# Kernel tuning notes

Hardware: AMD Instinct MI355X
Metric: run time of the kernel (lower is better)

Reference implementation:

```python
import jax, jax.numpy as jnp
import numpy as np

B, S, H, DK, DM = 8, 2048, 8, 64, 512  # batch, seq, heads, head dim, model dim
NEG = jnp.float32(-2**31)  # fill value for float32 per source


def setup_inputs() -> dict:
    key = jax.random.key(0)
    ks = jax.random.split(key, 8)
    q = jax.random.normal(ks[0], (B, S, DK), dtype=jnp.float32)
    k = jax.random.normal(ks[1], (B, S, DK), dtype=jnp.float32)
    v = jax.random.normal(ks[2], (B, S, DK), dtype=jnp.float32)
    mask = jax.random.randint(ks[3], (B, S, S), 0, 2).astype(jnp.float32)
    # torch Linear params stored as [in, out] for x @ W + b
    Wq = jax.random.normal(ks[4], (DK, H * DK), dtype=jnp.float32) / np.sqrt(DK).astype(np.float32)
    bq = jax.random.normal(ks[5], (H * DK,), dtype=jnp.float32) * 0.02
    Wo = jax.random.normal(ks[6], (H * DK, DM), dtype=jnp.float32) / np.sqrt(H * DK).astype(np.float32)
    bo = jax.random.normal(ks[7], (DM,), dtype=jnp.float32) * 0.02
    return {"q": q, "k": k, "v": v, "mask": mask, "Wq": Wq, "bq": bq, "Wo": Wo, "bo": bo}


def reference(q, k, v, mask, Wq, bq, Wo, bo):
    # Faithful to the source BUG: linear_q projects q, k AND v.
    def proj(x):
        b, s, _ = x.shape
        return (x @ Wq + bq).reshape(b, s, H, DK).transpose(2, 0, 1, 3)  # [H,B,S,DK]

    qh, kh, vh = proj(q), proj(k), proj(v)
    e = jnp.einsum('hbqd,hbkd->hbqk', qh, kh) / np.float32(np.sqrt(DK))  # [H,B,Sq,Sk]
    # source fills where ((mask-1).bool()==False), i.e. where mask == 1.0
    e = jnp.where(mask[None] == 1.0, NEG, e)
    a = jax.nn.softmax(e, axis=-1)
    y = jnp.einsum('hbqk,hbkd->hbqd', a, vh)          # [H,B,Sq,DK]
    y = y.transpose(1, 2, 0, 3).reshape(B, S, H * DK)  # [B,Sq,H*DK]
    return y @ Wo + bo
```

## Files before the change

### kernel.cpp

```cpp
#include <hip/hip_runtime.h>
#include <hip/hip_bf16.h>

#define BB 8
#define SS 2048
#define HD 512
#define DM 512

typedef __attribute__((ext_vector_type(8))) short short8;
typedef __attribute__((ext_vector_type(4))) short short4v;
typedef __attribute__((ext_vector_type(4))) float floatx4;

__device__ __forceinline__ unsigned cvt_pk_bf16(float a, float b) {
    unsigned r;
    asm("v_cvt_pk_bf16_f32 %0, %1, %2" : "=v"(r) : "v"(a), "v"(b));
    return r;
}

__device__ __forceinline__ short f2bf(float f) {
    return (short)(cvt_pk_bf16(f, f) & 0xFFFFu);
}

__device__ __forceinline__ uint2 pack4bf(float a, float b, float cc, float d) {
    return uint2{cvt_pk_bf16(a, b), cvt_pk_bf16(cc, d)};
}

__device__ __forceinline__ short4v pack4bf_s4(float a, float b, float cc, float d) {
    uint2 u = pack4bf(a, b, cc, d);
    short4v s;
    __builtin_memcpy(&s, &u, 8);
    return s;
}

__device__ __forceinline__ void async_copy16(const short* g, short* l) {
    __builtin_amdgcn_global_load_lds(
        (const __attribute__((address_space(1))) void*)g,
        (__attribute__((address_space(3))) void*)l, 16, 0, 0);
}

__global__ void maskbits_prep_kernel(const float* __restrict__ mask,
                                     unsigned long long* __restrict__ bits,
                                     const float* __restrict__ Wq,
                                     const float* __restrict__ Wo,
                                     short* __restrict__ WqT,
                                     short* __restrict__ WoT) {
    int bid = blockIdx.x;
    if (bid >= 32768) {
        int idx = (bid - 32768) * 256 + threadIdx.x;
        if (idx < HD * 64) {
            int o = idx >> 6, i = idx & 63;
            WqT[idx] = f2bf(Wq[i * HD + o]);
        }
        int o = idx >> 9, i = idx & 511;
        WoT[idx] = f2bf(Wo[i * DM + o]);
        return;
    }
    int gw = bid * 4 + (threadIdx.x >> 6);
    int lane = threadIdx.x & 63;
    size_t base = (size_t)gw * 256;
    float4 v = *(const float4*)(mask + base + (size_t)lane * 4);
    unsigned long long nib =
        (v.x == 1.0f ? 1ull : 0ull) | (v.y == 1.0f ? 2ull : 0ull) |
        (v.z == 1.0f ? 4ull : 0ull) | (v.w == 1.0f ? 8ull : 0ull);
    unsigned long long word = nib << (4 * (lane & 15));
    word |= __shfl_xor(word, 1);
    word |= __shfl_xor(word, 2);
    word |= __shfl_xor(word, 4);
    word |= __shfl_xor(word, 8);
    if ((lane & 15) == 0) bits[gw * 4 + (lane >> 4)] = word;
}

__global__ __launch_bounds__(256, 2) void proj_kernel(
    const float* __restrict__ qA, const float* __restrict__ kA,
    const float* __restrict__ vA, const short* __restrict__ WqT,
    const float* __restrict__ bq, short* __restrict__ qh,
    short* __restrict__ khS, short* __restrict__ vI) {
    const int bid = blockIdx.x;
    const int part = bid >> 9, sub = bid & 511;

    __shared__ __align__(16) short LDSbuf[2 * 128 * 80];
    short* As = LDSbuf;
    short* Bs = LDSbuf + 128 * 80;
    short* Cs = LDSbuf;

    const int tid = threadIdx.x, lane = tid & 63, w = tid >> 6;
    const int c = lane & 15, Q = lane >> 4;
    const int wm = w >> 1, wn = w & 1;

    int n0, m0, bz = 0;
    const float* Af32 = nullptr;
    if (part < 2) {
        n0 = (sub & 3) * 128;
        m0 = (sub >> 2) * 128;
        Af32 = part ? kA : qA;
    } else {
        n0 = (sub & 15) * 128;
        int rest = sub >> 4;
        m0 = (rest & 3) * 128;
        bz = rest >> 2;
    }

#pragma unroll
    for (int it = 0; it < 4; ++it) {
        int chunk = it * 256 + tid;
        int row = chunk >> 3, c8 = chunk & 7;
        if (part < 2) {
            const float* Af = Af32 + (size_t)(m0 + row) * 64 + c8 * 8;
            float4 lo = *(const float4*)Af;
            float4 hi = *(const float4*)(Af + 4);
            uint2 p0 = pack4bf(lo.x, lo.y, lo.z, lo.w);
            uint2 p1 = pack4bf(hi.x, hi.y, hi.z, hi.w);
            *(uint4*)&As[row * 80 + c8 * 8] = uint4{p0.x, p0.y, p1.x, p1.y};
            *(uint4*)&Bs[row * 80 + c8 * 8] =
                *(const uint4*)(WqT + (size_t)(n0 + row) * 64 + c8 * 8);
        } else {
            *(uint4*)&As[row * 80 + c8 * 8] =
                *(const uint4*)(WqT + (size_t)(m0 + row) * 64 + c8 * 8);
            const float* Bf = vA + (size_t)bz * 131072 +
                              (size_t)(n0 + row) * 64 + c8 * 8;
            float4 lo = *(const float4*)Bf;
            float4 hi = *(const float4*)(Bf + 4);
            uint2 p0 = pack4bf(lo.x, lo.y, lo.z, lo.w);
            uint2 p1 = pack4bf(hi.x, hi.y, hi.z, hi.w);
            *(uint4*)&Bs[row * 80 + c8 * 8] = uint4{p0.x, p0.y, p1.x, p1.y};
        }
    }
    __syncthreads();

    floatx4 acc[4][4] = {};
#pragma unroll
    for (int ks = 0; ks < 2; ++ks) {
        short8 af[4], bf[4];
#pragma unroll
        for (int mt = 0; mt < 4; ++mt)
            af[mt] = *(const short8*)&As[(wm * 64 + mt * 16 + c) * 80 + ks * 32 + 8 * Q];
#pragma unroll
        for (int nt = 0; nt < 4; ++nt)
            bf[nt] = *(const short8*)&Bs[(wn * 64 + nt * 16 + c) * 80 + ks * 32 + 8 * Q];
#pragma unroll
        for (int mt = 0; mt < 4; ++mt)
#pragma unroll
            for (int nt = 0; nt < 4; ++nt)
                acc[mt][nt] = __builtin_amdgcn_mfma_f32_16x16x32_bf16(
                    af[mt], bf[nt], acc[mt][nt], 0, 0, 0);
    }
    __syncthreads();

#pragma unroll
    for (int mt = 0; mt < 4; ++mt)
#pragma unroll
        for (int nt = 0; nt < 4; ++nt) {
            int cl = wn * 64 + nt * 16 + c;
#pragma unroll
            for (int r = 0; r < 4; ++r) {
                int rl = wm * 64 + mt * 16 + 4 * Q + r;
                if (part == 0) {
                    float val = (acc[mt][nt][r] + bq[n0 + cl]) * 0.18033688011f;
                    Cs[rl * 128 + cl] = f2bf(val);
                } else if (part == 1) {
                    float val = acc[mt][nt][r] + bq[n0 + cl];
                    int d = cl & 63, hh = cl >> 6;
                    Cs[rl * 128 + hh * 64 + (((d >> 3) ^ (rl & 7)) * 8) + (d & 7)] =
                        f2bf(val);
                } else {
                    float val = acc[mt][nt][r] + bq[m0 + rl];
                    int d = rl & 63, hl = rl >> 6;
                    int Jl = cl >> 5, kp = cl & 31;
                    int j = 4 * ((kp >> 4) & 1) + (kp & 3);
                    int Qm = (kp >> 2) & 3;
                    int slotm = Qm ^ ((d >> 1) & 3);
                    Cs[(hl * 4 + Jl) * 2048 + d * 32 + slotm * 8 + j] = f2bf(val);
                }
            }
        }
    __syncthreads();

#pragma unroll
    for (int p = 0; p < 8; ++p) {
        int c2 = p * 256 + tid;
        uint4 vchunk;
        size_t gaddr;
        if (part == 0) {
            int row = c2 >> 4, off16 = c2 & 15;
            vchunk = *(const uint4*)&Cs[row * 128 + off16 * 8];
            gaddr = (size_t)(m0 + row) * HD + n0 + off16 * 8;
            *(uint4*)(qh + gaddr) = vchunk;
        } else if (part == 1) {
            int sp = c2 >> 3, off = c2 & 7;
            int s = sp >> 1, hh = sp & 1;
            vchunk = *(const uint4*)&Cs[s * 128 + hh * 64 + off * 8];
            int grow = m0 + s;
            int b = grow >> 11, sg = grow & 2047;
            int hg = (n0 >> 6) + hh;
            gaddr = ((size_t)(b * 8 + hg)) * 131072 + (size_t)sg * 64 + off * 8;
            *(uint4*)(khS + gaddr) = vchunk;
        } else {
            int region = c2 >> 8, off = c2 & 255;
            int hl = region >> 2, Jl = region & 3;
            vchunk = *(const uint4*)&Cs[region * 2048 + off * 8];
            int hg = (m0 >> 6) + hl;
            int Jg = (n0 >> 5) + Jl;
            gaddr = ((size_t)(bz * 8 + hg)) * 131072 + (size_t)Jg * 2048 + off * 8;
            *(uint4*)(vI + gaddr) = vchunk;
        }
    }
}

template <int SMODE, bool BIAS_ROW, bool A_F32, bool B_F32>
__global__ __launch_bounds__(256, 2) void gemm_bt(
    const void* __restrict__ A_, int lda, long sA,
    const void* __restrict__ B_, int ldb, long sB,
    void* __restrict__ C, int ldc, long sC,
    const float* __restrict__ bias, int K, float alpha) {
    const int bz = blockIdx.z;
    const int m0 = blockIdx.y * 128, n0 = blockIdx.x * 128;
    __shared__ __align__(16) short As[128 * 80];
    __shared__ __align__(16) short Bs[128 * 80];
    const int tid = threadIdx.x, lane = tid & 63, w = tid >> 6;
    const int c = lane & 15, Q = lane >> 4;
    const int wm = w >> 1, wn = w & 1;
    floatx4 acc[4][4] = {};

    for (int k0 = 0; k0 < K; k0 += 64) {
#pragma unroll
        for (int it = 0; it < 4; ++it) {
            int chunk = it * 256 + tid;
            int row = chunk >> 3, c8 = chunk & 7;
            size_t aoff = (size_t)bz * sA + (size_t)(m0 + row) * lda + k0 + c8 * 8;
            size_t boff = (size_t)bz * sB + (size_t)(n0 + row) * ldb + k0 + c8 * 8;
            if (A_F32) {
                const float* Af = (const float*)A_ + aoff;
                float4 lo = *(const float4*)Af;
                float4 hi = *(const float4*)(Af + 4);
                uint2 p0 = pack4bf(lo.x, lo.y, lo.z, lo.w);
                uint2 p1 = pack4bf(hi.x, hi.y, hi.z, hi.w);
                *(uint4*)&As[row * 80 + c8 * 8] = uint4{p0.x, p0.y, p1.x, p1.y};
            } else {
                *(uint4*)&As[row * 80 + c8 * 8] = *(const uint4*)((const short*)A_ + aoff);
            }
            if (B_F32) {
                const float* Bf = (const float*)B_ + boff;
                float4 lo = *(const float4*)Bf;
                float4 hi = *(const float4*)(Bf + 4);
                uint2 p0 = pack4bf(lo.x, lo.y, lo.z, lo.w);
                uint2 p1 = pack4bf(hi.x, hi.y, hi.z, hi.w);
                *(uint4*)&Bs[row * 80 + c8 * 8] = uint4{p0.x, p0.y, p1.x, p1.y};
            } else {
                *(uint4*)&Bs[row * 80 + c8 * 8] = *(const uint4*)((const short*)B_ + boff);
            }
        }
        __syncthreads();
#pragma unroll
        for (int ks = 0; ks < 2; ++ks) {
            short8 af[4], bf[4];
#pragma unroll
            for (int mt = 0; mt < 4; ++mt)
                af[mt] = *(const short8*)&As[(wm * 64 + mt * 16 + c) * 80 + ks * 32 + 8 * Q];
#pragma unroll
            for (int nt = 0; nt < 4; ++nt)
                bf[nt] = *(const short8*)&Bs[(wn * 64 + nt * 16 + c) * 80 + ks * 32 + 8 * Q];
#pragma unroll
            for (int mt = 0; mt < 4; ++mt)
#pragma unroll
                for (int nt = 0; nt < 4; ++nt)
                    acc[mt][nt] = __builtin_amdgcn_mfma_f32_16x16x32_bf16(
                        af[mt], bf[nt], acc[mt][nt], 0, 0, 0);
        }
        __syncthreads();
    }
#pragma unroll
    for (int mt = 0; mt < 4; ++mt)
#pragma unroll
        for (int nt = 0; nt < 4; ++nt) {
            int col = n0 + wn * 64 + nt * 16 + c;
            float bc = BIAS_ROW ? 0.f : bias[col];
#pragma unroll
            for (int r = 0; r < 4; ++r) {
                int row = m0 + wm * 64 + mt * 16 + 4 * Q + r;
                float val = (acc[mt][nt][r] + (BIAS_ROW ? bias[row] : bc)) * alpha;
                if (SMODE == 0) {
                    ((float*)C)[(size_t)bz * sC + (size_t)row * ldc + col] = val;
                } else if (SMODE == 1) {
                    ((short*)C)[(size_t)bz * sC + (size_t)row * ldc + col] = f2bf(val);
                }
            }
        }
}

__global__ __launch_bounds__(512, 4) void fa_kernel(
    const short* __restrict__ qh, const short* __restrict__ khS,
    const short* __restrict__ vI, const unsigned* __restrict__ mbits,
    short* __restrict__ y) {
    const int id = blockIdx.x;
    const int xcd = id & 7, slot = id >> 3;
    const int qt = slot & 15;
    const int bh = (slot >> 4) * 8 + xcd;
    const int b = bh >> 3, h = bh & 7;
    const int tid = threadIdx.x, lane = tid & 63, w = tid >> 6;
    const int c = lane & 15, Q = lane >> 4;
    const int c7 = c & 7;
    const int vslot = Q ^ ((c >> 1) & 3);

    __shared__ __align__(16) short Ks[2 * 4096];
    __shared__ __align__(16) short Vs[2 * 4096];

    const short* kbase = khS + (size_t)bh * 131072;
    const short* vbase = vI + (size_t)bh * 131072;
    const int soff = tid * 8;

    async_copy16(kbase + soff, &Ks[soff]);
    async_copy16(vbase + soff, &Vs[soff]);

    const int qbase0 = qt * 128 + w * 16;
    const short* qb = qh + ((size_t)(b * SS + qbase0 + c)) * HD + h * 64;
    short8 qf0 = *(const short8*)(qb + 8 * Q);
    short8 qf1 = *(const short8*)(qb + 32 + 8 * Q);
    const unsigned* mrow = mbits + (size_t)(b * SS + qbase0 + c) * 64;

    short8 ones8;
#pragma unroll
    for (int i = 0; i < 8; ++i) ones8[i] = (short)0x3F80;

    floatx4 o[4] = {};
    floatx4 acc_l = {};

    __syncthreads();

    for (int kt2 = 0; kt2 < 16; ++kt2) {
        uint4 mr4 = *(const uint4*)(mrow + kt2 * 4);
#pragma unroll
        for (int hf = 0; hf < 2; ++hf) {
            const int kt = 2 * kt2 + hf;
            const int cb = hf * 4096;
            const int nb = (1 - hf) * 4096;
            const unsigned mlo = hf ? mr4.z : mr4.x;
            const unsigned mhi = hf ? mr4.w : mr4.y;

            if (kt < 31) {
                const short* kg = kbase + (kt + 1) * 4096;
                const short* vg = vbase + (kt + 1) * 4096;
                async_copy16(kg + soff, &Ks[nb + soff]);
                async_copy16(vg + soff, &Vs[nb + soff]);
            }

            short4v p4[4];
#pragma unroll
            for (int jt = 0; jt < 4; ++jt) {
                short8 k0 = *(const short8*)&Ks[cb + (16 * jt + c) * 64 + (Q ^ c7) * 8];
                short8 k1 = *(const short8*)&Ks[cb + (16 * jt + c) * 64 + ((Q + 4) ^ c7) * 8];
                floatx4 z = {};
                z = __builtin_amdgcn_mfma_f32_16x16x32_bf16(k0, qf0, z, 0, 0, 0);
                z = __builtin_amdgcn_mfma_f32_16x16x32_bf16(k1, qf1, z, 0, 0, 0);
                unsigned mwd = (jt & 2) ? mhi : mlo;
                unsigned nib = (mwd >> (((jt & 1) << 4) + 4 * Q)) & 0xFu;
                float p0 = (nib & 1u) ? 0.f : __builtin_amdgcn_exp2f(z[0]);
                float p1 = (nib & 2u) ? 0.f : __builtin_amdgcn_exp2f(z[1]);
                float p2 = (nib & 4u) ? 0.f : __builtin_amdgcn_exp2f(z[2]);
                float p3 = (nib & 8u) ? 0.f : __builtin_amdgcn_exp2f(z[3]);
                p4[jt] = pack4bf_s4(p0, p1, p2, p3);
            }

#pragma unroll
            for (int J = 0; J < 2; ++J) {
                short8 v8 = __builtin_shufflevector(p4[2 * J], p4[2 * J + 1],
                                                    0, 1, 2, 3, 4, 5, 6, 7);
                acc_l = __builtin_amdgcn_mfma_f32_16x16x32_bf16(v8, ones8, acc_l, 0, 0, 0);
#pragma unroll
                for (int nt = 0; nt < 4; ++nt) {
                    short8 vf = *(const short8*)&Vs[cb + J * 2048 + (16 * nt + c) * 32 + vslot * 8];
                    o[nt] = __builtin_amdgcn_mfma_f32_16x16x32_bf16(v8, vf, o[nt], 0, 0, 0);
                }
            }
            if (kt < 31) __syncthreads();
        }
    }

#pragma unroll
    for (int r = 0; r < 4; ++r) {
        float inv = 1.0f / acc_l[r];
        int row = qbase0 + 4 * Q + r;
#pragma unroll
        for (int nt = 0; nt < 4; ++nt)
            y[((size_t)(b * SS + row)) * HD + h * 64 + 16 * nt + c] =
                f2bf(o[nt][r] * inv);
    }
}

extern "C" void kernel_launch(void* const* d_in, const int* in_sizes, int n_in,
                              void* d_out, int out_size, void* d_ws, size_t ws_size,
                              hipStream_t stream) {
    const float* q    = (const float*)d_in[0];
    const float* k    = (const float*)d_in[1];
    const float* v    = (const float*)d_in[2];
    const float* mask = (const float*)d_in[3];
    const float* Wq   = (const float*)d_in[4];
    const float* bq   = (const float*)d_in[5];
    const float* Wo   = (const float*)d_in[6];
    const float* bo   = (const float*)d_in[7];

    char* ws = (char*)d_ws;
    const size_t MB = 1ull << 20;
    short* WqT = (short*)(ws + 0 * MB);
    short* WoT = (short*)(ws + 1 * MB);
    short* qh  = (short*)(ws + 8 * MB);
    short* khS = (short*)(ws + 24 * MB);
    short* vI  = (short*)(ws + 40 * MB);
    unsigned long long* bits = (unsigned long long*)(ws + 56 * MB);
    short* yb  = (short*)(ws + 60 * MB);
    float* out = (float*)d_out;

    maskbits_prep_kernel<<<33792, 256, 0, stream>>>(mask, bits, Wq, Wo, WqT, WoT);
    proj_kernel<<<dim3(1536, 1, 1), 256, 0, stream>>>(q, k, v, WqT, bq, qh, khS, vI);
    fa_kernel<<<dim3(1024, 1, 1), 512, 0, stream>>>(qh, khS, vI, (const unsigned*)bits, yb);
    gemm_bt<0, false, false, false><<<dim3(4, 128, 1), 256, 0, stream>>>(
        yb, 512, 0, WoT, 512, 0, (void*)out, 512, 0, bo, 512, 1.0f);
}
```

Baseline: 351.7 us.

## Fuse mask bit-packing and Wo transpose into projection kernel, use ballot

Result: slower. 414.5 us (+17.9%).

```diff
diff --git a/kernel.cpp b/kernel.cpp
--- a/kernel.cpp
+++ b/kernel.cpp
@@ -37,47 +37,46 @@
         (__attribute__((address_space(3))) void*)l, 16, 0, 0);
 }
 
-__global__ void maskbits_prep_kernel(const float* __restrict__ mask,
-                                     unsigned long long* __restrict__ bits,
-                                     const float* __restrict__ Wq,
-                                     const float* __restrict__ Wo,
-                                     short* __restrict__ WqT,
-                                     short* __restrict__ WoT) {
-    int bid = blockIdx.x;
-    if (bid >= 32768) {
-        int idx = (bid - 32768) * 256 + threadIdx.x;
-        if (idx < HD * 64) {
-            int o = idx >> 6, i = idx & 63;
-            WqT[idx] = f2bf(Wq[i * HD + o]);
-        }
-        int o = idx >> 9, i = idx & 511;
-        WoT[idx] = f2bf(Wo[i * DM + o]);
-        return;
-    }
-    int gw = bid * 4 + (threadIdx.x >> 6);
-    int lane = threadIdx.x & 63;
-    size_t base = (size_t)gw * 256;
-    float4 v = *(const float4*)(mask + base + (size_t)lane * 4);
-    unsigned long long nib =
-        (v.x == 1.0f ? 1ull : 0ull) | (v.y == 1.0f ? 2ull : 0ull) |
-        (v.z == 1.0f ? 4ull : 0ull) | (v.w == 1.0f ? 8ull : 0ull);
-    unsigned long long word = nib << (4 * (lane & 15));
-    word |= __shfl_xor(word, 1);
-    word |= __shfl_xor(word, 2);
-    word |= __shfl_xor(word, 4);
-    word |= __shfl_xor(word, 8);
-    if ((lane & 15) == 0) bits[gw * 4 + (lane >> 4)] = word;
-}
-
-__global__ __launch_bounds__(256, 2) void proj_kernel(
+__global__ void wqt_prep_kernel(const float* __restrict__ Wq,
+                                short* __restrict__ WqT) {
+    int idx = blockIdx.x * 256 + threadIdx.x;
+    int o = idx >> 6, i = idx & 63;
+    WqT[idx] = f2bf(Wq[i * HD + o]);
+}
+
+__global__ __launch_bounds__(256, 2) void fused_aux_kernel(
+    const float* __restrict__ mask, unsigned long long* __restrict__ bits,
+    const float* __restrict__ Wo, short* __restrict__ WoT,
     const float* __restrict__ qA, const float* __restrict__ kA,
     const float* __restrict__ vA, const short* __restrict__ WqT,
     const float* __restrict__ bq, short* __restrict__ qh,
     short* __restrict__ khS, short* __restrict__ vI) {
     const int bid = blockIdx.x;
-    const int part = bid >> 9, sub = bid & 511;
-
     __shared__ __align__(16) short LDSbuf[2 * 128 * 80];
+
+    if (bid < 16384) {
+        const int lane = threadIdx.x & 63, w = threadIdx.x >> 6;
+        const float* mrow = mask + (size_t)bid * 2048;
+        unsigned long long* brow = bits + (size_t)bid * 32;
+#pragma unroll
+        for (int i = 0; i < 8; ++i) {
+            int g = w * 8 + i;
+            float v = mrow[g * 64 + lane];
+            unsigned long long word = __ballot(v == 1.0f);
+            if (lane == 0) brow[g] = word;
+        }
+        return;
+    }
+    if (bid < 17408) {
+        int idx = (bid - 16384) * 256 + threadIdx.x;
+        int o = idx >> 9, i = idx & 511;
+        WoT[idx] = f2bf(Wo[i * DM + o]);
+        return;
+    }
+
+    const int pbid = bid - 17408;
+    const int part = pbid >> 9, sub = pbid & 511;
+
     short* As = LDSbuf;
     short* Bs = LDSbuf + 128 * 80;
     short* Cs = LDSbuf;
@@ -408,8 +407,9 @@
     short* yb  = (short*)(ws + 60 * MB);
     float* out = (float*)d_out;
 
-    maskbits_prep_kernel<<<33792, 256, 0, stream>>>(mask, bits, Wq, Wo, WqT, WoT);
-    proj_kernel<<<dim3(1536, 1, 1), 256, 0, stream>>>(q, k, v, WqT, bq, qh, khS, vI);
+    wqt_prep_kernel<<<128, 256, 0, stream>>>(Wq, WqT);
+    fused_aux_kernel<<<18944, 256, 0, stream>>>(
+        mask, bits, Wo, WoT, q, k, v, WqT, bq, qh, khS, vI);
     fa_kernel<<<dim3(1024, 1, 1), 512, 0, stream>>>(qh, khS, vI, (const unsigned*)bits, yb);
     gemm_bt<0, false, false, false><<<dim3(4, 128, 1), 256, 0, stream>>>(
         yb, 512, 0, WoT, 512, 0, (void*)out, 512, 0, bo, 512, 1.0f);
```
